# Optimization experiments

Measured on AMD Instinct MI355X. Metric: run time of the kernel, lower is better.

Reference implementation:

```python
import jax, jax.numpy as jnp
import numpy as np

N = 100000   # total nodes across batched graphs
E = 1600000  # total edges
B = 128      # number of graphs in batch
FEAT, H1, H2, P, OUT = 6, 128, 512, 2, 100
M0, M1 = 1024, 512  # MLP hidden dims
BN_EPS = 1e-5


def _lin_init(key, fan_in, fan_out):
    return jax.random.normal(key, (fan_in, fan_out), jnp.float32) / np.sqrt(fan_in)


def setup_inputs() -> dict:
    key = jax.random.key(0)
    ks = jax.random.split(key, 12)
    feat = jax.random.normal(ks[0], (N, FEAT), jnp.float32)
    prompt = jax.random.normal(ks[1], (B, P), jnp.float32)
    src = jax.random.randint(ks[2], (E,), 0, N, jnp.int32)
    dst = jax.random.randint(ks[3], (E,), 0, N, jnp.int32)
    graph_ids = jnp.sort(jax.random.randint(ks[4], (N,), 0, B, jnp.int32))
    return {
        "feat": feat, "prompt": prompt,
        "src": src, "dst": dst, "graph_ids": graph_ids,
        "W0": _lin_init(ks[5], FEAT, H1), "b0": jnp.zeros((H1,), jnp.float32),
        "W1": _lin_init(ks[6], H1, H2), "b1": jnp.zeros((H2,), jnp.float32),
        "Wp": _lin_init(ks[7], P, P), "bp": jnp.zeros((P,), jnp.float32),
        "Wm0": _lin_init(ks[8], H2 + P, M0), "bm0": jnp.zeros((M0,), jnp.float32),
        "g0": jnp.ones((M0,), jnp.float32), "be0": jnp.zeros((M0,), jnp.float32),
        "Wm1": _lin_init(ks[9], M0, M1), "bm1": jnp.zeros((M1,), jnp.float32),
        "g1": jnp.ones((M1,), jnp.float32), "be1": jnp.zeros((M1,), jnp.float32),
        "Wm2": _lin_init(ks[10], M1, OUT), "bm2": jnp.zeros((OUT,), jnp.float32),
    }


def reference(feat, prompt, src, dst, graph_ids,
              W0, b0, W1, b1, Wp, bp,
              Wm0, bm0, g0, be0, Wm1, bm1, g1, be1, Wm2, bm2):
    # GIN layer: neigh = sum_{j in N(i)} h_j ; h' = relu(Linear((1+eps)*h + neigh)), eps=0
    def gin(h, W, b):
        neigh = jax.ops.segment_sum(h[src], dst, num_segments=N)  # gather + scatter-add
        return jax.nn.relu((h + neigh) @ W + b)

    h = gin(feat, W0, b0)   # [N, 128]
    h = gin(h, W1, b1)      # [N, 512]

    pooled = jax.ops.segment_sum(h, graph_ids, num_segments=B)  # dgl.sum_nodes -> [B, 512]
    pr = prompt @ Wp + bp                                        # prompt_nn -> [B, 2]
    x = jnp.concatenate([pooled, pr], axis=-1)                   # [B, 514]

    # MLPBlock mode='NAD': Linear -> BatchNorm1d (batch stats) -> ReLU -> (Dropout p=0)
    def bn(z, g, be):
        m = z.mean(axis=0)
        v = z.var(axis=0)
        return g * (z - m) * jax.lax.rsqrt(v + BN_EPS) + be

    x = jax.nn.relu(bn(x @ Wm0 + bm0, g0, be0))
    x = jax.nn.relu(bn(x @ Wm1 + bm1, g1, be1))
    return x @ Wm2 + bm2  # [B, 100] XANES spectrum
```

## Files before the change

### kernel.cpp

```cpp
#include <hip/hip_runtime.h>
#include <hip/hip_bf16.h>

#define Nn 100000
#define Ee 1600000
#define Bb 128
#define XD 514
#define BN_EPS 1e-5f
#define SCAN_NB 196
#define NPART 8
#define PART_NODES 12500
#define PART_BLKS 2048
#define KC 128
#define NBIN_BLKS 2048
#define CH 784
#define PCAP 212992

using bf16x8 = __attribute__((ext_vector_type(8))) short;
using f32x4  = __attribute__((ext_vector_type(4))) float;

static __device__ __forceinline__ float grp32_sum(float v){
  v += __shfl_xor(v, 1);
  v += __shfl_xor(v, 2);
  v += __shfl_xor(v, 4);
  v += __shfl_xor(v, 8);
  v += __shfl_xor(v, 16);
  return v;
}

static __device__ __forceinline__ unsigned short f2bf(float f){
  unsigned u = __builtin_bit_cast(unsigned, f);
  unsigned r = (u + 0x7fffu + ((u >> 16) & 1u)) >> 16;
  return (unsigned short)r;
}

static __device__ __forceinline__ float bfl(unsigned u){ return __builtin_bit_cast(float, u << 16); }
static __device__ __forceinline__ float bfh(unsigned u){ return __builtin_bit_cast(float, u & 0xffff0000u); }

__global__ __launch_bounds__(256) void k_bin(const int* __restrict__ src, const int* __restrict__ dst,
                                             int* __restrict__ gCnt, int2* __restrict__ bins){
  __shared__ int sd[CH], ss[CH];
  __shared__ int hist[8], wbase[8], roff[8];
  int t = threadIdx.x;
  if (t < 8){ hist[t] = 0; roff[t] = 0; }
  __syncthreads();
  int e0 = blockIdx.x * CH;
  int e1 = e0 + CH; if (e1 > Ee) e1 = Ee;
  int n = e1 - e0;
  for (int i = t; i < n; i += 256){
    int d = __builtin_nontemporal_load(&dst[e0 + i]);
    int s = __builtin_nontemporal_load(&src[e0 + i]);
    sd[i] = d; ss[i] = s;
    atomicAdd(&hist[d / PART_NODES], 1);
  }
  __syncthreads();
  if (t < 8) wbase[t] = atomicAdd(&gCnt[t], hist[t]);
  __syncthreads();
  for (int i = t; i < n; i += 256){
    int d = sd[i];
    int p = d / PART_NODES;
    int off = atomicAdd(&roff[p], 1);
    bins[(size_t)p * PCAP + wbase[p] + off] = make_int2(d, ss[i]);
  }
}

__global__ __launch_bounds__(256) void k_count2(const int2* __restrict__ bins, const int* __restrict__ gCnt,
                                                int* __restrict__ deg){
  int p = blockIdx.x & (NPART-1);
  int nch = gridDim.x >> 3, chunk = blockIdx.x >> 3;
  int n = gCnt[p];
  const int2* bp = bins + (size_t)p * PCAP;
  for (int i = chunk*256 + threadIdx.x; i < n; i += nch*256){
    atomicAdd(&deg[bp[i].x], 1);
  }
}

__global__ __launch_bounds__(256) void k_scanA(const int* __restrict__ deg, int* __restrict__ bsum){
  __shared__ int red[256];
  int b = blockIdx.x, t = threadIdx.x;
  int i0 = b*512 + t;
  int v = 0;
  if (i0 < Nn) v += deg[i0];
  if (i0 + 256 < Nn) v += deg[i0+256];
  red[t] = v; __syncthreads();
  for (int off=128; off>0; off>>=1){
    if (t < off) red[t] += red[t+off];
    __syncthreads();
  }
  if (t==0) bsum[b] = red[0];
}

__global__ __launch_bounds__(256) void k_scanB(const int* __restrict__ bsum, int* __restrict__ boff,
                                               int* __restrict__ rowptrN, int nb){
  __shared__ int sA[256], sB[256];
  int t = threadIdx.x;
  int own = (t < nb) ? bsum[t] : 0;
  sA[t] = own; __syncthreads();
  int* s = sA; int* d = sB;
  #pragma unroll
  for (int off=1; off<256; off<<=1){
    int x = s[t]; if (t>=off) x += s[t-off];
    d[t] = x; __syncthreads();
    int* tmp = s; s = d; d = tmp;
  }
  int incl = s[t];
  if (t < nb) boff[t] = incl - own;
  if (t == 255) *rowptrN = incl;
}

__global__ __launch_bounds__(256) void k_scanC(const int* __restrict__ deg, const int* __restrict__ boff,
                                               int* __restrict__ rowptr){
  __shared__ int sA[256], sB[256];
  int b = blockIdx.x, t = threadIdx.x;
  int i0 = b*512 + 2*t;
  int a = (i0 < Nn) ? deg[i0] : 0;
  int c = (i0+1 < Nn) ? deg[i0+1] : 0;
  int s0 = a + c;
  sA[t] = s0; __syncthreads();
  int* s = sA; int* d = sB;
  #pragma unroll
  for (int off=1; off<256; off<<=1){
    int x = s[t]; if (t>=off) x += s[t-off];
    d[t] = x; __syncthreads();
    int* tmp = s; s = d; d = tmp;
  }
  int excl = s[t] - s0 + boff[b];
  if (i0 < Nn)   rowptr[i0]   = excl;
  if (i0+1 < Nn) rowptr[i0+1] = excl + a;
}

__global__ __launch_bounds__(256) void k_fill2(const int2* __restrict__ bins, const int* __restrict__ gCnt,
                                               int* __restrict__ cur, int* __restrict__ eidx){
  int p = blockIdx.x & (NPART-1);
  int nch = gridDim.x >> 3, chunk = blockIdx.x >> 3;
  int n = gCnt[p];
  const int2* bp = bins + (size_t)p * PCAP;
  for (int i = chunk*256 + threadIdx.x; i < n; i += nch*256){
    int2 e = bp[i];
    int q = atomicAdd(&cur[e.x], 1);
    eidx[q] = e.y;
  }
}

__global__ __launch_bounds__(256) void k_gin1(const float* __restrict__ feat, const int* __restrict__ rowptr,
                                              const int* __restrict__ eidx, float* __restrict__ x1){
  int i = blockIdx.x*256 + threadIdx.x;
  if (i >= Nn) return;
  float a0=feat[i*6+0], a1=feat[i*6+1], a2=feat[i*6+2],
        a3=feat[i*6+3], a4=feat[i*6+4], a5=feat[i*6+5];
  int beg = rowptr[i], end = rowptr[i+1];
  for (int j=beg; j<end; ++j){
    const float* f = feat + eidx[j]*6;
    a0+=f[0]; a1+=f[1]; a2+=f[2]; a3+=f[3]; a4+=f[4]; a5+=f[5];
  }
  float* o = x1 + i*6;
  o[0]=a0; o[1]=a1; o[2]=a2; o[3]=a3; o[4]=a4; o[5]=a5;
}

__global__ __launch_bounds__(256) void k_gin1mlp(const float* __restrict__ x1, const float* __restrict__ W0,
                                                 const float* __restrict__ b0, unsigned short* __restrict__ h1){
  __shared__ float sW[768];
  __shared__ float sb[128];
  int t = threadIdx.x;
  for (int i=t; i<768; i+=256) sW[i] = W0[i];
  if (t < 128) sb[t] = b0[t];
  __syncthreads();
  int row = blockIdx.x*2 + (t>>7);
  int c = t & 127;
  if (row >= Nn) return;
  const float* xr = x1 + row*6;
  float acc = sb[c];
  #pragma unroll
  for (int f=0; f<6; ++f) acc += xr[f]*sW[f*128+c];
  h1[row*128+c] = f2bf(fmaxf(acc, 0.f));
}

__global__ __launch_bounds__(256) void k_gather2(const unsigned short* __restrict__ h1,
                                                 const int* __restrict__ rowptr,
                                                 const int* __restrict__ eidx,
                                                 unsigned short* __restrict__ xb){
  int gt = blockIdx.x*256 + threadIdx.x;
  int node = gt >> 4;
  if (node >= Nn) return;
  int l = threadIdx.x & 15;
  int off = l*8;
  float a0,a1,a2,a3,a4,a5,a6,a7;
  {
    uint4 v = *(const uint4*)&h1[(size_t)node*128 + off];
    a0=bfl(v.x); a1=bfh(v.x); a2=bfl(v.y); a3=bfh(v.y);
    a4=bfl(v.z); a5=bfh(v.z); a6=bfl(v.w); a7=bfh(v.w);
  }
  int beg = rowptr[node], end = rowptr[node+1];
  int j = beg;
  for (; j+1 < end; j += 2){
    int s0 = eidx[j], s1 = eidx[j+1];
    uint4 u = *(const uint4*)&h1[(size_t)s0*128 + off];
    uint4 w = *(const uint4*)&h1[(size_t)s1*128 + off];
    a0 += bfl(u.x) + bfl(w.x);
    a1 += bfh(u.x) + bfh(w.x);
    a2 += bfl(u.y) + bfl(w.y);
    a3 += bfh(u.y) + bfh(w.y);
    a4 += bfl(u.z) + bfl(w.z);
    a5 += bfh(u.z) + bfh(w.z);
    a6 += bfl(u.w) + bfl(w.w);
    a7 += bfh(u.w) + bfh(w.w);
  }
  if (j < end){
    uint4 u = *(const uint4*)&h1[(size_t)eidx[j]*128 + off];
    a0 += bfl(u.x); a1 += bfh(u.x);
    a2 += bfl(u.y); a3 += bfh(u.y);
    a4 += bfl(u.z); a5 += bfh(u.z);
    a6 += bfl(u.w); a7 += bfh(u.w);
  }
  uint4 o;
  o.x = (unsigned)f2bf(a0) | ((unsigned)f2bf(a1) << 16);
  o.y = (unsigned)f2bf(a2) | ((unsigned)f2bf(a3) << 16);
  o.z = (unsigned)f2bf(a4) | ((unsigned)f2bf(a5) << 16);
  o.w = (unsigned)f2bf(a6) | ((unsigned)f2bf(a7) << 16);
  *(uint4*)&xb[(size_t)node*128 + off] = o;
}

__global__ __launch_bounds__(256) void k_packW(const float* __restrict__ W1, unsigned short* __restrict__ W1p){
  int t = blockIdx.x*256 + threadIdx.x;
  int l = t & 63;
  int s = (t >> 6) & 3;
  int f = t >> 8;
  int n = f*16 + (l & 15);
  int kb = s*32 + (l >> 4)*8;
  unsigned short o[8];
  #pragma unroll
  for (int e=0; e<8; ++e) o[e] = f2bf(W1[(kb+e)*512 + n]);
  uint4 pk;
  pk.x = (unsigned)o[0] | ((unsigned)o[1] << 16);
  pk.y = (unsigned)o[2] | ((unsigned)o[3] << 16);
  pk.z = (unsigned)o[4] | ((unsigned)o[5] << 16);
  pk.w = (unsigned)o[6] | ((unsigned)o[7] << 16);
  *(uint4*)&W1p[t*8] = pk;
}

__global__ __launch_bounds__(256) void k_gin2m(const unsigned short* __restrict__ xb,
                                               const unsigned short* __restrict__ W1p,
                                               const float* __restrict__ b1,
                                               const int* __restrict__ gids,
                                               float* __restrict__ pool){
  __shared__ float pool_lds[4][128];
  __shared__ int wgid[4];
  __shared__ int wuni_s[4];
  int w = threadIdx.x >> 6, l = threadIdx.x & 63;
  int wrow = blockIdx.x*128 + w*32;
  int fbase = blockIdx.y * 8;
  int kbase = (l >> 4) * 8;

  bf16x8 a[2][4];
  #pragma unroll
  for (int r=0; r<2; ++r){
    int arow = wrow + r*16 + (l & 15);
    if (arow > Nn-1) arow = Nn-1;
    const bf16x8* ap = (const bf16x8*)&xb[(size_t)arow*128 + kbase];
    #pragma unroll
    for (int s=0; s<4; ++s) a[r][s] = ap[s*4];
  }

  bool wvalid = wrow < Nn;
  bool wuni = (wrow + 31 < Nn) && (gids[wrow] == gids[wrow + 31]);
  if (l == 0){ wgid[w] = wuni ? gids[wrow] : -1; wuni_s[w] = wuni ? 1 : 0; }

  int rb[2], g0[2];
  bool uval[2];
  #pragma unroll
  for (int r=0; r<2; ++r){
    rb[r] = wrow + r*16 + ((l >> 4) & 3)*4;
    int i0 = rb[r], i3 = rb[r]+3;
    int c0 = i0 < Nn ? i0 : Nn-1;
    int c3 = i3 < Nn ? i3 : Nn-1;
    g0[r] = gids[c0];
    int g3 = gids[c3];
    uval[r] = (i3 < Nn) && (g0[r] == g3);
  }

  float acc_pool[8];
  #pragma unroll
  for (int i=0; i<8; ++i) acc_pool[i] = 0.f;

  const bf16x8* BpAll = (const bf16x8*)W1p;
  bf16x8 bcur[4];
  #pragma unroll
  for (int s=0; s<4; ++s) bcur[s] = BpAll[(fbase*4 + s)*64 + l];

  #pragma unroll
  for (int fi=0; fi<8; ++fi){
    int f = fbase + fi;
    bf16x8 bnext[4];
    if (fi < 7){
      #pragma unroll
      for (int s=0; s<4; ++s) bnext[s] = BpAll[((f+1)*4 + s)*64 + l];
    }
    f32x4 acc0 = {0.f,0.f,0.f,0.f};
    f32x4 acc1 = {0.f,0.f,0.f,0.f};
    #pragma unroll
    for (int s=0; s<4; ++s){
      acc0 = __builtin_amdgcn_mfma_f32_16x16x32_bf16(a[0][s], bcur[s], acc0, 0, 0, 0);
      acc1 = __builtin_amdgcn_mfma_f32_16x16x32_bf16(a[1][s], bcur[s], acc1, 0, 0, 0);
    }
    int col = f*16 + (l & 15);
    float bc = b1[col];
    if (wuni){
      float vsum = 0.f;
      #pragma unroll
      for (int r=0; r<2; ++r){
        f32x4 acc = r ? acc1 : acc0;
        float v = fmaxf(acc[0]+bc, 0.f) + fmaxf(acc[1]+bc, 0.f)
                + fmaxf(acc[2]+bc, 0.f) + fmaxf(acc[3]+bc, 0.f);
        v += __shfl_xor(v, 16);
        v += __shfl_xor(v, 32);
        vsum += v;
      }
      acc_pool[fi] = vsum;
    } else if (wvalid){
      #pragma unroll
      for (int r=0; r<2; ++r){
        f32x4 acc = r ? acc1 : acc0;
        float y0 = fmaxf(acc[0] + bc, 0.f);
        float y1 = fmaxf(acc[1] + bc, 0.f);
        float y2 = fmaxf(acc[2] + bc, 0.f);
        float y3 = fmaxf(acc[3] + bc, 0.f);
        int gg = g0[r];
        int ok = uval[r] ? 1 : 0;
        float v = y0 + y1 + y2 + y3;
        int gX  = __shfl_xor(gg, 16);
        int okX = __shfl_xor(ok, 16);
        ok = ok & okX & (gg == gX ? 1 : 0);
        float v2 = v + __shfl_xor(v, 16);
        int gY  = __shfl_xor(gg, 32);
        int okY = __shfl_xor(ok, 32);
        float v4 = v2 + __shfl_xor(v2, 32);
        ok = ok & okY & (gg == gY ? 1 : 0);
        if (ok){
          if (l < 16) atomicAdd(&pool[gg*XD + col], v4);
        } else {
          int base = rb[r];
          if (base   < Nn) atomicAdd(&pool[gids[base  ]*XD + col], y0);
          if (base+1 < Nn) atomicAdd(&pool[gids[base+1]*XD + col], y1);
          if (base+2 < Nn) atomicAdd(&pool[gids[base+2]*XD + col], y2);
          if (base+3 < Nn) atomicAdd(&pool[gids[base+3]*XD + col], y3);
        }
      }
    }
    if (fi < 7){
      #pragma unroll
      for (int s=0; s<4; ++s) bcur[s] = bnext[s];
    }
  }

  if (wuni && l < 16){
    #pragma unroll
    for (int fi=0; fi<8; ++fi) pool_lds[w][fi*16 + l] = acc_pool[fi];
  }
  __syncthreads();
  int t = threadIdx.x;
  if (t < 128){
    int cg = -1; float s = 0.f;
    #pragma unroll
    for (int ww=0; ww<4; ++ww){
      if (!wuni_s[ww]) continue;
      int g = wgid[ww];
      if (g != cg){
        if (cg >= 0) atomicAdd(&pool[cg*XD + fbase*16 + t], s);
        cg = g; s = 0.f;
      }
      s += pool_lds[ww][t];
    }
    if (cg >= 0) atomicAdd(&pool[cg*XD + fbase*16 + t], s);
  }
}

__global__ void k_pr(const float* __restrict__ prompt, const float* __restrict__ Wp,
                     const float* __restrict__ bp, float* __restrict__ xmlp){
  int t = threadIdx.x;
  if (t < 256){
    int r = t>>1, j = t&1;
    float v = prompt[r*2+0]*Wp[0*2+j] + prompt[r*2+1]*Wp[1*2+j] + bp[j];
    xmlp[r*XD + 512 + j] = v;
  }
}

__global__ __launch_bounds__(256) void k_lin(const float* __restrict__ X, const float* __restrict__ W,
                                             float* __restrict__ Zp, int K, int NC){
  __shared__ float xT[16][KC];
  int c = blockIdx.x*256 + threadIdx.x;
  int row0 = blockIdx.y*16;
  int k0 = blockIdx.z*KC;
  int kn = K - k0; if (kn > KC) kn = KC;
  if (kn == KC){
    int r = threadIdx.x >> 7;
    int kk = threadIdx.x & 127;
    #pragma unroll
    for (int i=0; i<8; ++i) xT[r + i*2][kk] = X[(size_t)(row0 + r + i*2)*K + k0 + kk];
  } else {
    for (int idx = threadIdx.x; idx < 16*kn; idx += 256){
      int r = idx / kn, kk = idx - r*kn;
      xT[r][kk] = X[(size_t)(row0+r)*K + k0 + kk];
    }
  }
  __syncthreads();
  float acc[16];
  #pragma unroll
  for (int r=0; r<16; ++r) acc[r] = 0.f;
  for (int kk=0; kk<kn; ++kk){
    float w = W[(size_t)(k0+kk)*NC + c];
    #pragma unroll
    for (int r=0; r<16; ++r) acc[r] += xT[r][kk]*w;
  }
  float* Zb = Zp + (size_t)blockIdx.z*128*NC;
  #pragma unroll
  for (int r=0; r<16; ++r) Zb[(size_t)(row0+r)*NC + c] = acc[r];
}

__global__ __launch_bounds__(256) void k_bnrelu(const float* __restrict__ Zp, const float* __restrict__ bias,
                                                const float* __restrict__ gamma, const float* __restrict__ beta,
                                                float* __restrict__ Y, int NC, int nk){
  int grp = threadIdx.x>>5, l32 = threadIdx.x&31;
  int col = blockIdx.x*8 + grp;
  int r0 = l32*4;
  float z0=0.f, z1=0.f, z2=0.f, z3=0.f;
  for (int j=0; j<nk; ++j){
    const float* Zb = Zp + (size_t)j*128*NC + col;
    z0 += Zb[(size_t)(r0+0)*NC];
    z1 += Zb[(size_t)(r0+1)*NC];
    z2 += Zb[(size_t)(r0+2)*NC];
    z3 += Zb[(size_t)(r0+3)*NC];
  }
  float bc = bias[col];
  z0+=bc; z1+=bc; z2+=bc; z3+=bc;
  float mean = grp32_sum(z0+z1+z2+z3) * (1.f/128.f);
  float d0=z0-mean, d1=z1-mean, d2=z2-mean, d3=z3-mean;
  float var = grp32_sum(d0*d0+d1*d1+d2*d2+d3*d3) * (1.f/128.f);
  float sc = gamma[col]*rsqrtf(var + BN_EPS);
  float bt = beta[col];
  Y[(size_t)(r0+0)*NC+col] = fmaxf(d0*sc+bt, 0.f);
  Y[(size_t)(r0+1)*NC+col] = fmaxf(d1*sc+bt, 0.f);
  Y[(size_t)(r0+2)*NC+col] = fmaxf(d2*sc+bt, 0.f);
  Y[(size_t)(r0+3)*NC+col] = fmaxf(d3*sc+bt, 0.f);
}

__global__ __launch_bounds__(128) void k_out(const float* __restrict__ y1, const float* __restrict__ W2,
                                             const float* __restrict__ b2, float* __restrict__ out){
  __shared__ float yr[512];
  int r = blockIdx.x;
  for (int k=threadIdx.x; k<512; k+=128) yr[k] = y1[r*512+k];
  __syncthreads();
  int c = threadIdx.x;
  if (c < 100){
    float a0=0.f, a1=0.f, a2=0.f, a3=0.f;
    for (int k=0; k<512; k+=4){
      a0 += yr[k+0]*W2[(k+0)*100+c];
      a1 += yr[k+1]*W2[(k+1)*100+c];
      a2 += yr[k+2]*W2[(k+2)*100+c];
      a3 += yr[k+3]*W2[(k+3)*100+c];
    }
    out[r*100+c] = b2[c] + ((a0+a1)+(a2+a3));
  }
}

extern "C" void kernel_launch(void* const* d_in, const int* in_sizes, int n_in,
                              void* d_out, int out_size, void* d_ws, size_t ws_size,
                              hipStream_t stream)
{
  const float* feat   = (const float*)d_in[0];
  const float* prompt = (const float*)d_in[1];
  const int*   src    = (const int*)d_in[2];
  const int*   dst    = (const int*)d_in[3];
  const int*   gids   = (const int*)d_in[4];
  const float* W0  = (const float*)d_in[5];
  const float* b0  = (const float*)d_in[6];
  const float* W1  = (const float*)d_in[7];
  const float* b1  = (const float*)d_in[8];
  const float* Wp  = (const float*)d_in[9];
  const float* bp  = (const float*)d_in[10];
  const float* Wm0 = (const float*)d_in[11];
  const float* bm0 = (const float*)d_in[12];
  const float* g0  = (const float*)d_in[13];
  const float* be0 = (const float*)d_in[14];
  const float* Wm1 = (const float*)d_in[15];
  const float* bm1 = (const float*)d_in[16];
  const float* g1  = (const float*)d_in[17];
  const float* be1 = (const float*)d_in[18];
  const float* Wm2 = (const float*)d_in[19];
  const float* bm2 = (const float*)d_in[20];
  float* out = (float*)d_out;

  char* p = (char*)d_ws;
  auto carve = [&](size_t bytes) -> void* {
    void* r = (void*)p;
    p += (bytes + 255) & ~(size_t)255;
    return r;
  };
  int*   deg    = (int*)carve((size_t)Nn*4);
  int*   rowptr = (int*)carve((size_t)(Nn+1)*4);
  int*   cur    = (int*)carve((size_t)Nn*4);
  int*   bsum   = (int*)carve(256*4);
  int*   boff   = (int*)carve(256*4);
  int*   gCnt   = (int*)carve(256*4);
  int*   eidx   = (int*)carve((size_t)Ee*4);
  float* x1     = (float*)carve((size_t)Nn*6*4);
  unsigned short* h1  = (unsigned short*)carve((size_t)Nn*128*2);
  unsigned short* xb  = (unsigned short*)carve((size_t)Nn*128*2);
  unsigned short* W1p = (unsigned short*)carve((size_t)128*512*2);
  float* xmlp   = (float*)carve((size_t)Bb*XD*4);
  float* y0     = (float*)carve((size_t)Bb*1024*4);
  float* y1     = (float*)carve((size_t)Bb*512*4);

  int2*  bins = (int2*)h1;
  float* Zp0 = (float*)eidx;
  float* Zp1 = (float*)x1;

  hipMemsetAsync(deg, 0, (size_t)Nn*4, stream);
  hipMemsetAsync(gCnt, 0, 8*4, stream);
  hipMemsetAsync(xmlp, 0, (size_t)Bb*XD*4, stream);

  k_packW<<<32, 256, 0, stream>>>(W1, W1p);

  k_bin<<<NBIN_BLKS, 256, 0, stream>>>(src, dst, gCnt, bins);
  k_count2<<<PART_BLKS, 256, 0, stream>>>(bins, gCnt, deg);
  k_scanA<<<SCAN_NB, 256, 0, stream>>>(deg, bsum);
  k_scanB<<<1, 256, 0, stream>>>(bsum, boff, rowptr + Nn, SCAN_NB);
  k_scanC<<<SCAN_NB, 256, 0, stream>>>(deg, boff, rowptr);
  hipMemcpyAsync(cur, rowptr, (size_t)Nn*4, hipMemcpyDeviceToDevice, stream);
  k_fill2<<<PART_BLKS, 256, 0, stream>>>(bins, gCnt, cur, eidx);

  k_gin1<<<(Nn+255)/256, 256, 0, stream>>>(feat, rowptr, eidx, x1);
  k_gin1mlp<<<Nn/2, 256, 0, stream>>>(x1, W0, b0, h1);

  k_gather2<<<(Nn*16+255)/256, 256, 0, stream>>>(h1, rowptr, eidx, xb);
  dim3 g2((Nn+127)/128, 4);
  k_gin2m<<<g2, 256, 0, stream>>>(xb, W1p, b1, gids, xmlp);

  k_pr<<<1, 256, 0, stream>>>(prompt, Wp, bp, xmlp);

  dim3 gl0(1024/256, 8, (XD + KC - 1)/KC);
  k_lin<<<gl0, 256, 0, stream>>>(xmlp, Wm0, Zp0, XD, 1024);
  k_bnrelu<<<1024/8, 256, 0, stream>>>(Zp0, bm0, g0, be0, y0, 1024, (XD + KC - 1)/KC);

  dim3 gl1(512/256, 8, 1024/KC);
  k_lin<<<gl1, 256, 0, stream>>>(y0, Wm1, Zp1, 1024, 512);
  k_bnrelu<<<512/8, 256, 0, stream>>>(Zp1, bm1, g1, be1, y1, 512, 1024/KC);

  k_out<<<Bb, 128, 0, stream>>>(y1, Wm2, bm2, out);
}
```

Before: 524.8 us.

## Replace global-atomic CSR build with fine-grained bins and per-bin LDS sort

Edges are now binned into 131 destination-node bins of 768 nodes each, rather than 8 partitions. Each binning block first sorts its chunk locally in shared memory so the global writes come out contiguous. Degree counting and the CSR fill then run one block per bin, using shared-memory histograms and a shared-memory counting sort, which replaces global atomics on deg and cur. This also removes the deg memset and the cur copy, but only 131 blocks run the per-bin kernels and each k_sort block needs about 56KB of LDS, which limits occupancy. It also assumes no bin ever holds more than PCAP2 edges.

```diff
diff --git a/kernel.cpp b/kernel.cpp
--- a/kernel.cpp
+++ b/kernel.cpp
@@ -7,13 +7,12 @@
 #define XD 514
 #define BN_EPS 1e-5f
 #define SCAN_NB 196
-#define NPART 8
-#define PART_NODES 12500
-#define PART_BLKS 2048
 #define KC 128
 #define NBIN_BLKS 2048
 #define CH 784
-#define PCAP 212992
+#define NBINS2 131
+#define BINN 768
+#define PCAP2 13312
 
 using bf16x8 = __attribute__((ext_vector_type(8))) short;
 using f32x4  = __attribute__((ext_vector_type(4))) float;
@@ -36,42 +35,68 @@
 static __device__ __forceinline__ float bfl(unsigned u){ return __builtin_bit_cast(float, u << 16); }
 static __device__ __forceinline__ float bfh(unsigned u){ return __builtin_bit_cast(float, u & 0xffff0000u); }
 
-__global__ __launch_bounds__(256) void k_bin(const int* __restrict__ src, const int* __restrict__ dst,
-                                             int* __restrict__ gCnt, int2* __restrict__ bins){
-  __shared__ int sd[CH], ss[CH];
-  __shared__ int hist[8], wbase[8], roff[8];
-  int t = threadIdx.x;
-  if (t < 8){ hist[t] = 0; roff[t] = 0; }
+
+__global__ __launch_bounds__(256) void k_bin2(const int* __restrict__ src, const int* __restrict__ dst,
+                                              int* __restrict__ gCnt, int2* __restrict__ bins){
+  __shared__ int sd[CH], ss[CH], od[CH], os[CH];
+  __shared__ int hist[NBINS2], wbase[NBINS2], roff[NBINS2], lbase[NBINS2];
+  __shared__ int sA[256], sBv[256];
+  int t = threadIdx.x;
+  for (int b=t; b<NBINS2; b+=256){ hist[b]=0; roff[b]=0; }
   __syncthreads();
   int e0 = blockIdx.x * CH;
   int e1 = e0 + CH; if (e1 > Ee) e1 = Ee;
   int n = e1 - e0;
-  for (int i = t; i < n; i += 256){
-    int d = __builtin_nontemporal_load(&dst[e0 + i]);
-    int s = __builtin_nontemporal_load(&src[e0 + i]);
-    sd[i] = d; ss[i] = s;
-    atomicAdd(&hist[d / PART_NODES], 1);
-  }
-  __syncthreads();
-  if (t < 8) wbase[t] = atomicAdd(&gCnt[t], hist[t]);
-  __syncthreads();
-  for (int i = t; i < n; i += 256){
+  for (int i=t; i<n; i+=256){
+    int d = __builtin_nontemporal_load(&dst[e0+i]);
+    int s = __builtin_nontemporal_load(&src[e0+i]);
+    sd[i]=d; ss[i]=s;
+    atomicAdd(&hist[d/BINN], 1);
+  }
+  __syncthreads();
+  int own = (t < NBINS2) ? hist[t] : 0;
+  sA[t] = own; __syncthreads();
+  int* sp = sA; int* dp = sBv;
+  #pragma unroll
+  for (int off=1; off<256; off<<=1){
+    int x = sp[t]; if (t>=off) x += sp[t-off];
+    dp[t] = x; __syncthreads();
+    int* tmp = sp; sp = dp; dp = tmp;
+  }
+  if (t < NBINS2){
+    lbase[t] = sp[t] - own;
+    if (own > 0) wbase[t] = atomicAdd(&gCnt[t], own);
+  }
+  __syncthreads();
+  for (int i=t; i<n; i+=256){
     int d = sd[i];
-    int p = d / PART_NODES;
-    int off = atomicAdd(&roff[p], 1);
-    bins[(size_t)p * PCAP + wbase[p] + off] = make_int2(d, ss[i]);
-  }
-}
-
-__global__ __launch_bounds__(256) void k_count2(const int2* __restrict__ bins, const int* __restrict__ gCnt,
-                                                int* __restrict__ deg){
-  int p = blockIdx.x & (NPART-1);
-  int nch = gridDim.x >> 3, chunk = blockIdx.x >> 3;
-  int n = gCnt[p];
-  const int2* bp = bins + (size_t)p * PCAP;
-  for (int i = chunk*256 + threadIdx.x; i < n; i += nch*256){
-    atomicAdd(&deg[bp[i].x], 1);
-  }
+    int b = d / BINN;
+    int loc = atomicAdd(&roff[b], 1);
+    int pos = lbase[b] + loc;
+    od[pos] = d; os[pos] = ss[i];
+  }
+  __syncthreads();
+  for (int i=t; i<n; i+=256){
+    int d = od[i];
+    int b = d / BINN;
+    bins[(size_t)b*PCAP2 + wbase[b] + (i - lbase[b])] = make_int2(d, os[i]);
+  }
+}
+
+__global__ __launch_bounds__(256) void k_deg(const int2* __restrict__ bins, const int* __restrict__ gCnt,
+                                             int* __restrict__ deg){
+  __shared__ int lhist[BINN];
+  int b = blockIdx.x;
+  int nb = b*BINN;
+  int nn = Nn - nb; if (nn > BINN) nn = BINN;
+  int t = threadIdx.x;
+  for (int j=t; j<nn; j+=256) lhist[j]=0;
+  __syncthreads();
+  int n = gCnt[b];
+  const int2* bp = bins + (size_t)b*PCAP2;
+  for (int i=t; i<n; i+=256) atomicAdd(&lhist[bp[i].x - nb], 1);
+  __syncthreads();
+  for (int j=t; j<nn; j+=256) deg[nb+j] = lhist[j];
 }
 
 __global__ __launch_bounds__(256) void k_scanA(const int* __restrict__ deg, int* __restrict__ bsum){
@@ -128,17 +153,29 @@
   if (i0+1 < Nn) rowptr[i0+1] = excl + a;
 }
 
-__global__ __launch_bounds__(256) void k_fill2(const int2* __restrict__ bins, const int* __restrict__ gCnt,
-                                               int* __restrict__ cur, int* __restrict__ eidx){
-  int p = blockIdx.x & (NPART-1);
-  int nch = gridDim.x >> 3, chunk = blockIdx.x >> 3;
-  int n = gCnt[p];
-  const int2* bp = bins + (size_t)p * PCAP;
-  for (int i = chunk*256 + threadIdx.x; i < n; i += nch*256){
+__global__ __launch_bounds__(256) void k_sort(const int2* __restrict__ bins, const int* __restrict__ gCnt,
+                                              const int* __restrict__ rowptr, int* __restrict__ eidx){
+  __shared__ int lrp[BINN+1];
+  __shared__ int cnt[BINN];
+  __shared__ int sorted[PCAP2];
+  int b = blockIdx.x;
+  int nb = b*BINN;
+  int nn = Nn - nb; if (nn > BINN) nn = BINN;
+  int t = threadIdx.x;
+  for (int j=t; j<=nn; j+=256) lrp[j] = rowptr[nb+j];
+  for (int j=t; j<nn; j+=256) cnt[j] = 0;
+  __syncthreads();
+  int base0 = lrp[0];
+  int n = gCnt[b];
+  const int2* bp = bins + (size_t)b*PCAP2;
+  for (int i=t; i<n; i+=256){
     int2 e = bp[i];
-    int q = atomicAdd(&cur[e.x], 1);
-    eidx[q] = e.y;
-  }
+    int dl = e.x - nb;
+    int pos = lrp[dl] - base0 + atomicAdd(&cnt[dl], 1);
+    sorted[pos] = e.y;
+  }
+  __syncthreads();
+  for (int i=t; i<n; i+=256) eidx[base0+i] = sorted[i];
 }
 
 __global__ __launch_bounds__(256) void k_gin1(const float* __restrict__ feat, const int* __restrict__ rowptr,
@@ -496,7 +533,6 @@
   };
   int*   deg    = (int*)carve((size_t)Nn*4);
   int*   rowptr = (int*)carve((size_t)(Nn+1)*4);
-  int*   cur    = (int*)carve((size_t)Nn*4);
   int*   bsum   = (int*)carve(256*4);
   int*   boff   = (int*)carve(256*4);
   int*   gCnt   = (int*)carve(256*4);
@@ -513,19 +549,17 @@
   float* Zp0 = (float*)eidx;
   float* Zp1 = (float*)x1;
 
-  hipMemsetAsync(deg, 0, (size_t)Nn*4, stream);
-  hipMemsetAsync(gCnt, 0, 8*4, stream);
+  hipMemsetAsync(gCnt, 0, 256*4, stream);
   hipMemsetAsync(xmlp, 0, (size_t)Bb*XD*4, stream);
 
   k_packW<<<32, 256, 0, stream>>>(W1, W1p);
 
-  k_bin<<<NBIN_BLKS, 256, 0, stream>>>(src, dst, gCnt, bins);
-  k_count2<<<PART_BLKS, 256, 0, stream>>>(bins, gCnt, deg);
+  k_bin2<<<NBIN_BLKS, 256, 0, stream>>>(src, dst, gCnt, bins);
+  k_deg<<<NBINS2, 256, 0, stream>>>(bins, gCnt, deg);
   k_scanA<<<SCAN_NB, 256, 0, stream>>>(deg, bsum);
   k_scanB<<<1, 256, 0, stream>>>(bsum, boff, rowptr + Nn, SCAN_NB);
   k_scanC<<<SCAN_NB, 256, 0, stream>>>(deg, boff, rowptr);
-  hipMemcpyAsync(cur, rowptr, (size_t)Nn*4, hipMemcpyDeviceToDevice, stream);
-  k_fill2<<<PART_BLKS, 256, 0, stream>>>(bins, gCnt, cur, eidx);
+  k_sort<<<NBINS2, 256, 0, stream>>>(bins, gCnt, rowptr, eidx);
 
   k_gin1<<<(Nn+255)/256, 256, 0, stream>>>(feat, rowptr, eidx, x1);
   k_gin1mlp<<<Nn/2, 256, 0, stream>>>(x1, W0, b0, h1);
```

Measured after the change: 436.8 us. 16.8% less time.
